# Optimization experiments

Hardware: AMD Instinct MI355X
Metric: run time of the kernel (lower is better)

## Reference

```python
import jax, jax.numpy as jnp
import numpy as np

B, S, D, FF, E = 4, 2048, 1024, 4096, 8


def setup_inputs() -> dict:
    key = jax.random.key(0)
    ks = jax.random.split(key, 6)
    scale_r = 1.0 / np.sqrt(D)
    return {
        "x": jax.random.normal(ks[0], (B, S, D), dtype=jnp.float32),
        "W_router": jax.random.normal(ks[1], (D, E), dtype=jnp.float32) * scale_r,
        "W1": jax.random.normal(ks[2], (E, D, FF), dtype=jnp.float32) * (1.0 / np.sqrt(D)),
        "b1": jnp.zeros((E, FF), dtype=jnp.float32),
        "W2": jax.random.normal(ks[3], (E, FF, D), dtype=jnp.float32) * (1.0 / np.sqrt(FF)),
        "b2": jnp.zeros((E, D), dtype=jnp.float32),
    }


def reference(x, W_router, W1, b1, W2, b2):
    # Router: softmax over experts, top-2, renormalize the 2 gates with softmax
    logits = jnp.einsum("bsd,de->bse", x, W_router)          # [B,S,E]
    probs = jax.nn.softmax(logits, axis=-1)
    top_vals, top_idx = jax.lax.top_k(probs, 2)               # [B,S,2]
    gates2 = jax.nn.softmax(top_vals, axis=-1)                # [B,S,2]

    num_experts = W1.shape[0]
    out = jnp.zeros_like(x)
    # Faithful masked-dense MoE: each expert runs over all tokens (input masked),
    # output scaled by its gate (0 for non-selected tokens).
    for i in range(num_experts):
        sel = (top_idx == i)                                  # [B,S,2] bool
        mask = jnp.any(sel, axis=-1, keepdims=True).astype(x.dtype)  # [B,S,1]
        xi = x * mask
        h = jax.nn.gelu(jnp.einsum("bsd,df->bsf", xi, W1[i]) + b1[i], approximate=False)
        yi = jnp.einsum("bsf,fd->bsd", h, W2[i]) + b2[i]
        g = jnp.sum(gates2 * sel.astype(x.dtype), axis=-1, keepdims=True)  # [B,S,1]
        out = out + yi * g
    return out
```

## Files before the change

### kernel.cpp

```cpp
#include <hip/hip_runtime.h>
#include <hip/hip_bf16.h>
#include <math.h>

#define NEXP 8
#define DDIM 1024
#define FFDIM 4096
#define NTOK 8192
#define NSLOT (NTOK * 2)
#define BM 128
#define BN 128
#define BK 64
#define MAXT ((NSLOT / BM) + NEXP)

typedef __attribute__((ext_vector_type(8))) __bf16 bf16x8;
typedef __attribute__((ext_vector_type(4))) __bf16 bf16x4;
typedef __attribute__((ext_vector_type(4))) float f32x4;

union BF8 { __bf16 b[8]; uint4 u; bf16x8 v; };

typedef const __attribute__((address_space(1))) void* gptr1_t;
typedef __attribute__((address_space(3))) void* lptr3_t;
__device__ __forceinline__ void gll16(const void* g, void* l) {
    __builtin_amdgcn_global_load_lds((gptr1_t)g, (lptr3_t)l, 16, 0, 0);
}

__device__ __forceinline__ float gelu_fast(float v) {
    float vv = v * v;
    float ex = __expf(v * fmaf(0.0713548162726f, vv, 1.59576912161f));
    float s = __builtin_amdgcn_rcpf(ex + 1.0f);
    return v * (1.0f - s);
}

__device__ __forceinline__ int swz(int row, int colb) {
    return row * 128 + (colb ^ ((row & 7) << 4));
}

__device__ __forceinline__ int xcd_logical(int bid, int nwg) {
    if (nwg & 7) return bid;
    return (bid & 7) * (nwg >> 3) + (bid >> 3);
}

__global__ __launch_bounds__(256)
void router_kernel(const float* __restrict__ x, const float* __restrict__ Wr,
                   __bf16* __restrict__ xb, int write_xb,
                   int* __restrict__ idx2, float* __restrict__ gates2,
                   int* __restrict__ counts)
{
    int tid = threadIdx.x;
    int t = blockIdx.x * 4 + (tid >> 6);
    int lane = tid & 63;
    const float* xr = x + (size_t)t * DDIM;

    float acc[NEXP];
#pragma unroll
    for (int e = 0; e < NEXP; ++e) acc[e] = 0.f;

#pragma unroll
    for (int i = 0; i < 2; ++i) {
        int d0 = i * 512 + lane * 8;
        float4 a = *(const float4*)(xr + d0);
        float4 b = *(const float4*)(xr + d0 + 4);
        float vals[8] = {a.x, a.y, a.z, a.w, b.x, b.y, b.z, b.w};
#pragma unroll
        for (int q = 0; q < 8; ++q) {
            const float* wrow = Wr + (size_t)(d0 + q) * NEXP;
#pragma unroll
            for (int e = 0; e < NEXP; ++e) acc[e] += vals[q] * wrow[e];
        }
        if (write_xb) {
            BF8 pk;
#pragma unroll
            for (int q = 0; q < 8; ++q) pk.b[q] = (__bf16)vals[q];
            *(uint4*)(xb + (size_t)t * DDIM + d0) = pk.u;
        }
    }
#pragma unroll
    for (int e = 0; e < NEXP; ++e) {
        float v = acc[e];
        for (int off = 32; off > 0; off >>= 1) v += __shfl_xor(v, off, 64);
        acc[e] = v;
    }
    if (lane == 0) {
        float mx = acc[0];
#pragma unroll
        for (int e = 1; e < NEXP; ++e) mx = fmaxf(mx, acc[e]);
        float p[NEXP]; float s = 0.f;
#pragma unroll
        for (int e = 0; e < NEXP; ++e) { p[e] = expf(acc[e] - mx); s += p[e]; }
        float inv = 1.f / s;
#pragma unroll
        for (int e = 0; e < NEXP; ++e) p[e] *= inv;
        int i1 = 0; float p1 = p[0];
#pragma unroll
        for (int e = 1; e < NEXP; ++e) if (p[e] > p1) { p1 = p[e]; i1 = e; }
        int i2 = -1; float p2 = -1.f;
#pragma unroll
        for (int e = 0; e < NEXP; ++e) {
            if (e == i1) continue;
            if (p[e] > p2) { p2 = p[e]; i2 = e; }
        }
        float u = expf(p2 - p1);
        float den = 1.f + u;
        idx2[2 * t] = i1; idx2[2 * t + 1] = i2;
        gates2[2 * t] = 1.f / den; gates2[2 * t + 1] = u / den;
        atomicAdd(&counts[i1], 1);
        atomicAdd(&counts[i2], 1);
    }
}

__global__ __launch_bounds__(256)
void offsets_kernel(const int* __restrict__ counts, int* __restrict__ offsets,
                    int* __restrict__ cursors, int* __restrict__ tiletab)
{
    __shared__ int soff[NEXP], stile[NEXP + 1];
    int tid = threadIdx.x;
    if (tid == 0) {
        int off = 0, tt = 0;
        for (int e = 0; e < NEXP; ++e) {
            soff[e] = off; stile[e] = tt;
            int c = counts[e];
            off += c; tt += (c + BM - 1) / BM;
        }
        stile[NEXP] = tt;
    }
    __syncthreads();
    if (tid < NEXP) { offsets[tid] = soff[tid]; cursors[tid] = 0; }
    int total = stile[NEXP];
    for (int i = tid; i < MAXT; i += 256) {
        if (i < total) {
            int e = 0;
            while (stile[e + 1] <= i) ++e;
            tiletab[2 * i] = e; tiletab[2 * i + 1] = i - stile[e];
        } else {
            tiletab[2 * i] = -1; tiletab[2 * i + 1] = 0;
        }
    }
}

__global__ __launch_bounds__(256)
void fill_kernel(const int* __restrict__ idx2, const float* __restrict__ gates2,
                 const int* __restrict__ offsets, int* __restrict__ cursors,
                 int* __restrict__ perm, float* __restrict__ gate_slot,
                 int* __restrict__ tslot)
{
    int t = blockIdx.x * 256 + threadIdx.x;
    if (t >= NTOK) return;
#pragma unroll
    for (int s = 0; s < 2; ++s) {
        int e = idx2[2 * t + s];
        int pos = atomicAdd(&cursors[e], 1);
        int slot = offsets[e] + pos;
        perm[slot] = t;
        gate_slot[slot] = gates2[2 * t + s];
        tslot[2 * t + s] = slot;
    }
}

__global__ __launch_bounds__(256)
void convert_w_kernel(const float* __restrict__ W1, const float* __restrict__ W2,
                      __bf16* __restrict__ W1T, __bf16* __restrict__ W2T)
{
    __shared__ float tile[64][133];
    int y = blockIdx.y;
    const float* W; __bf16* WT; int K, N, e;
    if (y < NEXP) { W = W1; WT = W1T; K = DDIM; N = FFDIM; e = y; }
    else          { W = W2; WT = W2T; K = FFDIM; N = DDIM; e = y - NEXP; }
    int ktiles = K >> 6;
    int nt = blockIdx.x / ktiles;
    int kt = blockIdx.x % ktiles;
    const float* We = W + (size_t)e * K * N + (size_t)(kt * 64) * N + nt * 128;
    int tid = threadIdx.x;

    int kr = tid >> 5;
    int n4 = (tid & 31) * 4;
#pragma unroll
    for (int i = 0; i < 8; ++i) {
        int k = kr + i * 8;
        float4 v = *(const float4*)(We + (size_t)k * N + n4);
        tile[k][n4] = v.x; tile[k][n4 + 1] = v.y;
        tile[k][n4 + 2] = v.z; tile[k][n4 + 3] = v.w;
    }
    __syncthreads();

    char* dstb = (char*)WT + ((((size_t)e * (N >> 7) + nt) * ktiles + kt) << 14);
#pragma unroll
    for (int it = 0; it < 4; ++it) {
        int off = it * 4096 + tid * 16;
        int r = off >> 7;
        int s = (off >> 4) & 7;
        int gi = s ^ (r & 7);
        BF8 pk;
#pragma unroll
        for (int q = 0; q < 8; ++q) pk.b[q] = (__bf16)tile[gi * 8 + q][r];
        *(uint4*)(dstb + off) = pk.u;
    }
}

__device__ __forceinline__ bool tile_header(const int* counts, const int* offsets,
                                            const int* tiletab, int e_arg, int c_arg, int CH,
                                            int tile_idx,
                                            int& e, int& start, int& cnt, int& hbase, int& row0,
                                            int& rows_here)
{
    int rowtile;
    if (e_arg >= 0) {
        e = e_arg;
        int cbase = c_arg * CH;
        cnt = counts[e] - cbase;
        if (cnt <= 0) return false;
        if (cnt > CH) cnt = CH;
        start = offsets[e] + cbase;
        rowtile = tile_idx;
        hbase = start;
    } else {
        e = tiletab[2 * tile_idx];
        if (e < 0) return false;
        rowtile = tiletab[2 * tile_idx + 1];
        start = offsets[e];
        cnt = counts[e];
        hbase = 0;
    }
    row0 = rowtile * BM;
    if (row0 >= cnt) return false;
    rows_here = cnt - row0;
    if (rows_here > BM) rows_here = BM;
    return true;
}

__global__ __launch_bounds__(256)
void gemm1_fast(const __bf16* __restrict__ xb, const __bf16* __restrict__ W1T,
                const float* __restrict__ b1,
                const int* __restrict__ perm, const int* __restrict__ counts,
                const int* __restrict__ offsets, const int* __restrict__ tiletab,
                __bf16* __restrict__ H, int e_arg, int c_arg, int CH)
{
    __shared__ __align__(16) char smem[(BM + BN) * 128];
    char* As = smem;
    char* Bs = smem + BM * 128;

    int e, start, cnt, hbase, row0, rows_here;
    if (!tile_header(counts, offsets, tiletab, e_arg, c_arg, CH, blockIdx.y,
                     e, start, cnt, hbase, row0, rows_here))
        return;

    const float* b1e = b1 + (size_t)e * FFDIM;
    int nt = blockIdx.x;
    int n0 = nt * BN;
    const char* bsrc = (const char*)W1T + ((((size_t)e * (FFDIM >> 7) + nt) * (DDIM >> 6)) << 14);

    int tid = threadIdx.x;
    int lane = tid & 63;
    int wid = tid >> 6;
    int wm = wid >> 1, wn = wid & 1;
    int lr = lane & 15, lhi = lane >> 4;

    int ar = tid >> 1, ach = tid & 1;
    int token = -1;
    if (ar < rows_here) token = perm[start + row0 + ar];
    const __bf16* arow = xb + (size_t)(token < 0 ? 0 : token) * DDIM + ach * 32;

    const char* bwave = bsrc + wid * 4096 + lane * 16;
    char* bldsb = Bs + wid * 4096;

    f32x4 acc[4][4] = {};

    for (int kt = 0; kt < DDIM / BK; ++kt) {
        __syncthreads();
#pragma unroll
        for (int j = 0; j < 4; ++j)
            gll16(bwave + ((size_t)kt << 14) + j * 1024, bldsb + j * 1024);
        {
            uint4 v[4];
            if (token >= 0) {
                const uint4* p = (const uint4*)(arow + kt * BK);
#pragma unroll
                for (int i = 0; i < 4; ++i) v[i] = p[i];
            } else {
#pragma unroll
                for (int i = 0; i < 4; ++i) v[i] = make_uint4(0u, 0u, 0u, 0u);
            }
#pragma unroll
            for (int i = 0; i < 4; ++i)
                *(uint4*)(As + swz(ar, ach * 64 + i * 16)) = v[i];
        }
        __syncthreads();

#pragma unroll
        for (int kk = 0; kk < 2; ++kk) {
            bf16x8 af[4], bfr[4];
#pragma unroll
            for (int m = 0; m < 4; ++m)
                af[m] = *(const bf16x8*)(As + swz(wm * 64 + m * 16 + lr, kk * 64 + lhi * 16));
#pragma unroll
            for (int n = 0; n < 4; ++n)
                bfr[n] = *(const bf16x8*)(Bs + swz(wn * 64 + n * 16 + lr, kk * 64 + lhi * 16));
#pragma unroll
            for (int m = 0; m < 4; ++m)
#pragma unroll
                for (int n = 0; n < 4; ++n)
                    acc[m][n] = __builtin_amdgcn_mfma_f32_16x16x32_bf16(af[m], bfr[n], acc[m][n], 0, 0, 0);
        }
    }

    float bias[4];
#pragma unroll
    for (int n = 0; n < 4; ++n) bias[n] = b1e[n0 + wn * 64 + n * 16 + lr];

#pragma unroll
    for (int m = 0; m < 4; ++m) {
        int rbase = wm * 64 + m * 16 + lhi * 4;
#pragma unroll
        for (int j = 0; j < 4; ++j) {
            int rl = rbase + j;
            if (rl < rows_here) {
                __bf16* hr = H + (size_t)(start + row0 + rl - hbase) * FFDIM + n0 + wn * 64;
#pragma unroll
                for (int n = 0; n < 4; ++n) {
                    float v = acc[m][n][j] + bias[n];
                    hr[n * 16 + lr] = (__bf16)gelu_fast(v);
                }
            }
        }
    }
}

__global__ __launch_bounds__(256)
void gemm2_fast(const __bf16* __restrict__ H, const __bf16* __restrict__ W2T,
                const float* __restrict__ b2,
                const int* __restrict__ perm, const float* __restrict__ gate_slot,
                const int* __restrict__ counts, const int* __restrict__ offsets,
                const int* __restrict__ tiletab,
                float* __restrict__ out, __bf16* __restrict__ Y, int use_y,
                int e_arg, int c_arg, int CH)
{
    __shared__ __align__(16) char smem[(BM + BN) * 128];
    char* As = smem;
    char* Bs = smem + BM * 128;

    const int NTN = DDIM / BN;
    int tile_idx, nt;
    if (e_arg >= 0) { nt = blockIdx.x; tile_idx = blockIdx.y; }
    else {
        int L = xcd_logical(blockIdx.x, gridDim.x);
        nt = L % NTN;
        tile_idx = L / NTN;
    }

    int e, start, cnt, hbase, row0, rows_here;
    if (!tile_header(counts, offsets, tiletab, e_arg, c_arg, CH, tile_idx,
                     e, start, cnt, hbase, row0, rows_here))
        return;

    const float* b2e = b2 + (size_t)e * DDIM;
    int n0 = nt * BN;
    const char* bsrc = (const char*)W2T + ((((size_t)e * (DDIM >> 7) + nt) * (FFDIM >> 6)) << 14);

    int tid = threadIdx.x;
    int lane = tid & 63;
    int wid = tid >> 6;
    int wm = wid >> 1, wn = wid & 1;
    int lr = lane & 15, lhi = lane >> 4;

    int ar = tid >> 1, ach = tid & 1;
    bool aval = (ar < rows_here);
    const __bf16* hrow = H + (size_t)(aval ? (start + row0 + ar - hbase) : 0) * FFDIM + ach * 32;

    const char* bwave = bsrc + wid * 4096 + lane * 16;
    char* bldsb = Bs + wid * 4096;

    f32x4 acc[4][4] = {};

    for (int kt = 0; kt < FFDIM / BK; ++kt) {
        __syncthreads();
#pragma unroll
        for (int j = 0; j < 4; ++j)
            gll16(bwave + ((size_t)kt << 14) + j * 1024, bldsb + j * 1024);
        {
            uint4 v[4];
            if (aval) {
                const uint4* p = (const uint4*)(hrow + kt * BK);
#pragma unroll
                for (int i = 0; i < 4; ++i) v[i] = p[i];
            } else {
#pragma unroll
                for (int i = 0; i < 4; ++i) v[i] = make_uint4(0u, 0u, 0u, 0u);
            }
#pragma unroll
            for (int i = 0; i < 4; ++i)
                *(uint4*)(As + swz(ar, ach * 64 + i * 16)) = v[i];
        }
        __syncthreads();

#pragma unroll
        for (int kk = 0; kk < 2; ++kk) {
            bf16x8 af[4], bfr[4];
#pragma unroll
            for (int m = 0; m < 4; ++m)
                af[m] = *(const bf16x8*)(As + swz(wm * 64 + m * 16 + lr, kk * 64 + lhi * 16));
#pragma unroll
            for (int n = 0; n < 4; ++n)
                bfr[n] = *(const bf16x8*)(Bs + swz(wn * 64 + n * 16 + lr, kk * 64 + lhi * 16));
#pragma unroll
            for (int m = 0; m < 4; ++m)
#pragma unroll
                for (int n = 0; n < 4; ++n)
                    acc[m][n] = __builtin_amdgcn_mfma_f32_16x16x32_bf16(af[m], bfr[n], acc[m][n], 0, 0, 0);
        }
    }

    float bias[4];
#pragma unroll
    for (int n = 0; n < 4; ++n) bias[n] = b2e[n0 + wn * 64 + n * 16 + lr];

#pragma unroll
    for (int m = 0; m < 4; ++m) {
        int rbase = wm * 64 + m * 16 + lhi * 4;
#pragma unroll
        for (int j = 0; j < 4; ++j) {
            int rl = rbase + j;
            if (rl < rows_here) {
                int slot = start + row0 + rl;
                float g = gate_slot[slot];
                if (use_y) {
                    __bf16* yrow = Y + (size_t)slot * DDIM + n0 + wn * 64;
#pragma unroll
                    for (int n = 0; n < 4; ++n)
                        yrow[n * 16 + lr] = (__bf16)((acc[m][n][j] + bias[n]) * g);
                } else {
                    int token = perm[slot];
                    float* orow = out + (size_t)token * DDIM + n0 + wn * 64;
#pragma unroll
                    for (int n = 0; n < 4; ++n)
                        atomicAdd(orow + n * 16 + lr, (acc[m][n][j] + bias[n]) * g);
                }
            }
        }
    }
}

__global__ __launch_bounds__(256)
void combine_kernel(const __bf16* __restrict__ Y, const int* __restrict__ tslot,
                    float* __restrict__ out)
{
    int t = blockIdx.x;
    int c = threadIdx.x * 4;
    int sa = tslot[2 * t], sb = tslot[2 * t + 1];
    bf16x4 a = *(const bf16x4*)(Y + (size_t)sa * DDIM + c);
    bf16x4 b = *(const bf16x4*)(Y + (size_t)sb * DDIM + c);
    float4 r;
    r.x = (float)a[0] + (float)b[0];
    r.y = (float)a[1] + (float)b[1];
    r.z = (float)a[2] + (float)b[2];
    r.w = (float)a[3] + (float)b[3];
    *(float4*)(out + (size_t)t * DDIM + c) = r;
}

__global__ __launch_bounds__(256)
void gemm1_legacy(const float* __restrict__ x, const float* __restrict__ W1,
                  const float* __restrict__ b1,
                  const int* __restrict__ perm, const int* __restrict__ counts,
                  const int* __restrict__ offsets, const int* __restrict__ tiletab,
                  __bf16* __restrict__ H, int e_arg, int c_arg, int CH)
{
    __shared__ __align__(16) char smem[(BM + BN) * 128];
    char* As = smem;
    char* Bs = smem + BM * 128;

    int e, start, cnt, hbase, row0, rows_here;
    if (!tile_header(counts, offsets, tiletab, e_arg, c_arg, CH, blockIdx.y,
                     e, start, cnt, hbase, row0, rows_here))
        return;

    const float* W1e = W1 + (size_t)e * DDIM * FFDIM;
    const float* b1e = b1 + (size_t)e * FFDIM;
    int n0 = blockIdx.x * BN;

    int tid = threadIdx.x;
    int lane = tid & 63;
    int wid = tid >> 6;
    int wm = wid >> 1, wn = wid & 1;
    int lr = lane & 15, lhi = lane >> 4;

    int ar = tid >> 1, ach = tid & 1;
    int token = -1;
    if (ar < rows_here) token = perm[start + row0 + ar];
    const float* arow = x + (size_t)(token < 0 ? 0 : token) * DDIM + ach * 32;

    int bn = tid & 127, bkh = tid >> 7;
    const float* bcol = W1e + (size_t)bkh * 32 * FFDIM + n0 + bn;

    f32x4 acc[4][4] = {};

    for (int k0 = 0; k0 < DDIM; k0 += BK) {
        __syncthreads();
        {
            BF8 pk[4];
            if (token >= 0) {
                const float4* p = (const float4*)(arow + k0);
#pragma unroll
                for (int i = 0; i < 4; ++i) {
                    float4 v0 = p[2 * i], v1 = p[2 * i + 1];
                    pk[i].b[0] = (__bf16)v0.x; pk[i].b[1] = (__bf16)v0.y;
                    pk[i].b[2] = (__bf16)v0.z; pk[i].b[3] = (__bf16)v0.w;
                    pk[i].b[4] = (__bf16)v1.x; pk[i].b[5] = (__bf16)v1.y;
                    pk[i].b[6] = (__bf16)v1.z; pk[i].b[7] = (__bf16)v1.w;
                }
            } else {
#pragma unroll
                for (int i = 0; i < 4; ++i) pk[i].u = make_uint4(0u, 0u, 0u, 0u);
            }
#pragma unroll
            for (int i = 0; i < 4; ++i)
                *(uint4*)(As + swz(ar, ach * 64 + i * 16)) = pk[i].u;
        }
        {
            float f[32];
            const float* p = bcol + (size_t)k0 * FFDIM;
#pragma unroll
            for (int j = 0; j < 32; ++j) f[j] = p[(size_t)j * FFDIM];
#pragma unroll
            for (int i = 0; i < 4; ++i) {
                BF8 pk;
#pragma unroll
                for (int q = 0; q < 8; ++q) pk.b[q] = (__bf16)f[i * 8 + q];
                *(uint4*)(Bs + swz(bn, bkh * 64 + i * 16)) = pk.u;
            }
        }
        __syncthreads();

#pragma unroll
        for (int kk = 0; kk < 2; ++kk) {
            bf16x8 af[4], bfr[4];
#pragma unroll
            for (int m = 0; m < 4; ++m)
                af[m] = *(const bf16x8*)(As + swz(wm * 64 + m * 16 + lr, kk * 64 + lhi * 16));
#pragma unroll
            for (int n = 0; n < 4; ++n)
                bfr[n] = *(const bf16x8*)(Bs + swz(wn * 64 + n * 16 + lr, kk * 64 + lhi * 16));
#pragma unroll
            for (int m = 0; m < 4; ++m)
#pragma unroll
                for (int n = 0; n < 4; ++n)
                    acc[m][n] = __builtin_amdgcn_mfma_f32_16x16x32_bf16(af[m], bfr[n], acc[m][n], 0, 0, 0);
        }
    }

    float bias[4];
#pragma unroll
    for (int n = 0; n < 4; ++n) bias[n] = b1e[n0 + wn * 64 + n * 16 + lr];

#pragma unroll
    for (int m = 0; m < 4; ++m) {
        int rbase = wm * 64 + m * 16 + lhi * 4;
#pragma unroll
        for (int j = 0; j < 4; ++j) {
            int rl = rbase + j;
            if (rl < rows_here) {
                __bf16* hr = H + (size_t)(start + row0 + rl - hbase) * FFDIM + n0 + wn * 64;
#pragma unroll
                for (int n = 0; n < 4; ++n) {
                    float v = acc[m][n][j] + bias[n];
                    hr[n * 16 + lr] = (__bf16)gelu_fast(v);
                }
            }
        }
    }
}

__global__ __launch_bounds__(256)
void gemm2_legacy(const __bf16* __restrict__ H, const float* __restrict__ W2,
                  const float* __restrict__ b2,
                  const int* __restrict__ perm, const float* __restrict__ gate_slot,
                  const int* __restrict__ counts, const int* __restrict__ offsets,
                  const int* __restrict__ tiletab,
                  float* __restrict__ out, int e_arg, int c_arg, int CH)
{
    __shared__ __align__(16) char smem[(BM + BN) * 128];
    char* As = smem;
    char* Bs = smem + BM * 128;

    int e, start, cnt, hbase, row0, rows_here;
    if (!tile_header(counts, offsets, tiletab, e_arg, c_arg, CH, blockIdx.y,
                     e, start, cnt, hbase, row0, rows_here))
        return;

    const float* W2e = W2 + (size_t)e * FFDIM * DDIM;
    const float* b2e = b2 + (size_t)e * DDIM;
    int n0 = blockIdx.x * BN;

    int tid = threadIdx.x;
    int lane = tid & 63;
    int wid = tid >> 6;
    int wm = wid >> 1, wn = wid & 1;
    int lr = lane & 15, lhi = lane >> 4;

    int ar = tid >> 1, ach = tid & 1;
    bool aval = (ar < rows_here);
    const __bf16* hrow = H + (size_t)(aval ? (start + row0 + ar - hbase) : 0) * FFDIM + ach * 32;

    int bn = tid & 127, bkh = tid >> 7;
    const float* bcol = W2e + (size_t)bkh * 32 * DDIM + n0 + bn;

    f32x4 acc[4][4] = {};

    for (int k0 = 0; k0 < FFDIM; k0 += BK) {
        __syncthreads();
        {
            uint4 v[4];
            if (aval) {
                const uint4* p = (const uint4*)(hrow + k0);
#pragma unroll
                for (int i = 0; i < 4; ++i) v[i] = p[i];
            } else {
#pragma unroll
                for (int i = 0; i < 4; ++i) v[i] = make_uint4(0u, 0u, 0u, 0u);
            }
#pragma unroll
            for (int i = 0; i < 4; ++i)
                *(uint4*)(As + swz(ar, ach * 64 + i * 16)) = v[i];
        }
        {
            float f[32];
            const float* p = bcol + (size_t)k0 * DDIM;
#pragma unroll
            for (int j = 0; j < 32; ++j) f[j] = p[(size_t)j * DDIM];
#pragma unroll
            for (int i = 0; i < 4; ++i) {
                BF8 pk;
#pragma unroll
                for (int q = 0; q < 8; ++q) pk.b[q] = (__bf16)f[i * 8 + q];
                *(uint4*)(Bs + swz(bn, bkh * 64 + i * 16)) = pk.u;
            }
        }
        __syncthreads();

#pragma unroll
        for (int kk = 0; kk < 2; ++kk) {
            bf16x8 af[4], bfr[4];
#pragma unroll
            for (int m = 0; m < 4; ++m)
                af[m] = *(const bf16x8*)(As + swz(wm * 64 + m * 16 + lr, kk * 64 + lhi * 16));
#pragma unroll
            for (int n = 0; n < 4; ++n)
                bfr[n] = *(const bf16x8*)(Bs + swz(wn * 64 + n * 16 + lr, kk * 64 + lhi * 16));
#pragma unroll
            for (int m = 0; m < 4; ++m)
#pragma unroll
                for (int n = 0; n < 4; ++n)
                    acc[m][n] = __builtin_amdgcn_mfma_f32_16x16x32_bf16(af[m], bfr[n], acc[m][n], 0, 0, 0);
        }
    }

    float bias[4];
#pragma unroll
    for (int n = 0; n < 4; ++n) bias[n] = b2e[n0 + wn * 64 + n * 16 + lr];

#pragma unroll
    for (int m = 0; m < 4; ++m) {
        int rbase = wm * 64 + m * 16 + lhi * 4;
#pragma unroll
        for (int j = 0; j < 4; ++j) {
            int rl = rbase + j;
            if (rl < rows_here) {
                int slot = start + row0 + rl;
                int token = perm[slot];
                float g = gate_slot[slot];
                float* orow = out + (size_t)token * DDIM + n0 + wn * 64;
#pragma unroll
                for (int n = 0; n < 4; ++n) {
                    float v = (acc[m][n][j] + bias[n]) * g;
                    atomicAdd(orow + n * 16 + lr, v);
                }
            }
        }
    }
}

extern "C" void kernel_launch(void* const* d_in, const int* in_sizes, int n_in,
                              void* d_out, int out_size, void* d_ws, size_t ws_size,
                              hipStream_t stream)
{
    const float* x  = (const float*)d_in[0];
    const float* Wr = (const float*)d_in[1];
    const float* W1 = (const float*)d_in[2];
    const float* b1 = (const float*)d_in[3];
    const float* W2 = (const float*)d_in[4];
    const float* b2 = (const float*)d_in[5];
    float* out = (float*)d_out;

    char* ws = (char*)d_ws;
    int* counts   = (int*)ws;
    int* offsets  = counts + 8;
    int* cursors  = offsets + 8;
    int* tiletab  = cursors + 8;
    int* idx2     = tiletab + 2 * MAXT;
    float* gates2 = (float*)(idx2 + 2 * NTOK);
    int* perm     = (int*)(gates2 + 2 * NTOK);
    float* gate_slot = (float*)(perm + NSLOT);
    int* tslot    = (int*)(gate_slot + NSLOT);
    char* hraw = (char*)(tslot + 2 * NTOK);
    size_t small_end = (((size_t)(hraw - ws)) + 255) & ~(size_t)255;

    __bf16* xb  = (__bf16*)(ws + small_end);
    __bf16* W1T = xb + (size_t)NTOK * DDIM;
    __bf16* W2T = W1T + (size_t)NEXP * DDIM * FFDIM;
    __bf16* Hf  = W2T + (size_t)NEXP * FFDIM * DDIM;
    __bf16* Y   = W1T;
    size_t fast_off = small_end + ((size_t)NTOK * DDIM + 2 * (size_t)NEXP * DDIM * FFDIM) * 2;
    size_t availHf = ws_size > fast_off ? ws_size - fast_off : 0;
    size_t need_H = (size_t)NSLOT * FFDIM * 2;
    bool have_w = availHf >= (size_t)BM * FFDIM * 2 * 8;

    hipMemsetAsync(counts, 0, 8 * sizeof(int), stream);

    router_kernel<<<NTOK / 4, 256, 0, stream>>>(x, Wr, xb, have_w ? 1 : 0,
                                                idx2, gates2, counts);
    if (have_w) {
        convert_w_kernel<<<dim3(512, 2 * NEXP), 256, 0, stream>>>(W1, W2, W1T, W2T);
    }
    offsets_kernel<<<1, 256, 0, stream>>>(counts, offsets, cursors, tiletab);
    fill_kernel<<<NTOK / 256, 256, 0, stream>>>(idx2, gates2, offsets, cursors, perm, gate_slot, tslot);

    if (have_w && availHf >= need_H) {
        dim3 g1(FFDIM / BN, MAXT, 1);
        gemm1_fast<<<g1, 256, 0, stream>>>(xb, W1T, b1, perm, counts, offsets, tiletab, Hf, -1, 0, 0);
        gemm2_fast<<<(DDIM / BN) * MAXT, 256, 0, stream>>>(Hf, W2T, b2, perm, gate_slot, counts,
                                                           offsets, tiletab, out, Y, 1, -1, 0, 0);
        combine_kernel<<<NTOK, 256, 0, stream>>>(Y, tslot, out);
    } else if (have_w) {
        hipMemsetAsync(d_out, 0, (size_t)out_size * sizeof(float), stream);
        long long chl = (long long)((availHf / ((size_t)FFDIM * 2)) / BM) * BM;
        int CH = (int)(chl > 4096 ? 4096 : chl);
        int nchunk = (NSLOT + CH - 1) / CH;
        for (int e = 0; e < NEXP; ++e) {
            for (int c = 0; c < nchunk; ++c) {
                dim3 g1(FFDIM / BN, CH / BM, 1);
                gemm1_fast<<<g1, 256, 0, stream>>>(xb, W1T, b1, perm, counts, offsets, tiletab, Hf, e, c, CH);
                dim3 g2(DDIM / BN, CH / BM, 1);
                gemm2_fast<<<g2, 256, 0, stream>>>(Hf, W2T, b2, perm, gate_slot, counts, offsets, tiletab,
                                                   out, (__bf16*)nullptr, 0, e, c, CH);
            }
        }
    } else {
        hipMemsetAsync(d_out, 0, (size_t)out_size * sizeof(float), stream);
        __bf16* H = (__bf16*)(ws + small_end);
        size_t avail = ws_size > small_end ? ws_size - small_end : 0;
        if (avail >= need_H) {
            dim3 g1(FFDIM / BN, MAXT, 1);
            gemm1_legacy<<<g1, 256, 0, stream>>>(x, W1, b1, perm, counts, offsets, tiletab, H, -1, 0, 0);
            dim3 g2(DDIM / BN, MAXT, 1);
            gemm2_legacy<<<g2, 256, 0, stream>>>(H, W2, b2, perm, gate_slot, counts, offsets, tiletab, out, -1, 0, 0);
        } else {
            long long chl = (long long)((avail / ((size_t)FFDIM * 2)) / BM) * BM;
            int CH = (int)(chl > 2048 ? 2048 : chl);
            if (CH >= BM) {
                int nchunk = (NSLOT + CH - 1) / CH;
                for (int e = 0; e < NEXP; ++e) {
                    for (int c = 0; c < nchunk; ++c) {
                        dim3 g1(FFDIM / BN, CH / BM, 1);
                        gemm1_legacy<<<g1, 256, 0, stream>>>(x, W1, b1, perm, counts, offsets, tiletab, H, e, c, CH);
                        dim3 g2(DDIM / BN, CH / BM, 1);
                        gemm2_legacy<<<g2, 256, 0, stream>>>(H, W2, b2, perm, gate_slot, counts, offsets, tiletab, out, e, c, CH);
                    }
                }
            }
        }
    }
}
```

Measured before the change: 766.6 us.

## Widen fast GEMM tiles to 128x256 with per-wave 128x64 output

Both fast expert GEMMs now compute 128x256 output tiles instead of 128x128. Each wave covers all 128 rows and a 64-column slice, so the A tile is reused across twice as many columns and half as many blocks reload A. The cost is twice the accumulator registers per wave (8x4 MFMA tiles), 48KB of shared memory and fewer blocks in the grid, which may cut occupancy and wave-level parallelism.

```diff
diff --git a/kernel.cpp b/kernel.cpp
--- a/kernel.cpp
+++ b/kernel.cpp
@@ -8,7 +8,7 @@
 #define NTOK 8192
 #define NSLOT (NTOK * 2)
 #define BM 128
-#define BN 128
+#define BN2 256
 #define BK 64
 #define MAXT ((NSLOT / BM) + NEXP)
 
@@ -234,9 +234,9 @@
                 const int* __restrict__ offsets, const int* __restrict__ tiletab,
                 __bf16* __restrict__ H, int e_arg, int c_arg, int CH)
 {
-    __shared__ __align__(16) char smem[(BM + BN) * 128];
+    __shared__ __align__(16) char smem[48 * 1024];
     char* As = smem;
-    char* Bs = smem + BM * 128;
+    char* Bs = smem + 16384;
 
     int e, start, cnt, hbase, row0, rows_here;
     if (!tile_header(counts, offsets, tiletab, e_arg, c_arg, CH, blockIdx.y,
@@ -244,14 +244,16 @@
         return;
 
     const float* b1e = b1 + (size_t)e * FFDIM;
-    int nt = blockIdx.x;
-    int n0 = nt * BN;
-    const char* bsrc = (const char*)W1T + ((((size_t)e * (FFDIM >> 7) + nt) * (DDIM >> 6)) << 14);
+    int ntb = blockIdx.x;
+    int n0 = ntb * BN2;
+    const int ktiles = DDIM >> 6;
+    const char* bpanel = (const char*)W1T +
+        ((((size_t)e * (FFDIM >> 7) + 2 * ntb) * ktiles) << 14);
+    const size_t substride = (size_t)ktiles << 14;
 
     int tid = threadIdx.x;
     int lane = tid & 63;
     int wid = tid >> 6;
-    int wm = wid >> 1, wn = wid & 1;
     int lr = lane & 15, lhi = lane >> 4;
 
     int ar = tid >> 1, ach = tid & 1;
@@ -259,16 +261,19 @@
     if (ar < rows_here) token = perm[start + row0 + ar];
     const __bf16* arow = xb + (size_t)(token < 0 ? 0 : token) * DDIM + ach * 32;
 
-    const char* bwave = bsrc + wid * 4096 + lane * 16;
-    char* bldsb = Bs + wid * 4096;
-
-    f32x4 acc[4][4] = {};
+    int bsub = wid >> 1;
+    const char* bsrcw = bpanel + bsub * substride + (wid & 1) * 8192 + lane * 16;
+    char* bldsw = Bs + wid * 8192;
+    const char* bfrag = Bs + bsub * 16384;
+    int bro = (wid & 1) * 64;
+
+    f32x4 acc[8][4] = {};
 
     for (int kt = 0; kt < DDIM / BK; ++kt) {
         __syncthreads();
 #pragma unroll
-        for (int j = 0; j < 4; ++j)
-            gll16(bwave + ((size_t)kt << 14) + j * 1024, bldsb + j * 1024);
+        for (int j = 0; j < 8; ++j)
+            gll16(bsrcw + ((size_t)kt << 14) + j * 1024, bldsw + j * 1024);
         {
             uint4 v[4];
             if (token >= 0) {
@@ -287,33 +292,32 @@
 
 #pragma unroll
         for (int kk = 0; kk < 2; ++kk) {
-            bf16x8 af[4], bfr[4];
-#pragma unroll
-            for (int m = 0; m < 4; ++m)
-                af[m] = *(const bf16x8*)(As + swz(wm * 64 + m * 16 + lr, kk * 64 + lhi * 16));
+            bf16x8 bfr[4];
 #pragma unroll
             for (int n = 0; n < 4; ++n)
-                bfr[n] = *(const bf16x8*)(Bs + swz(wn * 64 + n * 16 + lr, kk * 64 + lhi * 16));
-#pragma unroll
-            for (int m = 0; m < 4; ++m)
+                bfr[n] = *(const bf16x8*)(bfrag + swz(bro + n * 16 + lr, kk * 64 + lhi * 16));
+#pragma unroll
+            for (int m = 0; m < 8; ++m) {
+                bf16x8 af = *(const bf16x8*)(As + swz(m * 16 + lr, kk * 64 + lhi * 16));
 #pragma unroll
                 for (int n = 0; n < 4; ++n)
-                    acc[m][n] = __builtin_amdgcn_mfma_f32_16x16x32_bf16(af[m], bfr[n], acc[m][n], 0, 0, 0);
+                    acc[m][n] = __builtin_amdgcn_mfma_f32_16x16x32_bf16(af, bfr[n], acc[m][n], 0, 0, 0);
+            }
         }
     }
 
     float bias[4];
 #pragma unroll
-    for (int n = 0; n < 4; ++n) bias[n] = b1e[n0 + wn * 64 + n * 16 + lr];
-
-#pragma unroll
-    for (int m = 0; m < 4; ++m) {
-        int rbase = wm * 64 + m * 16 + lhi * 4;
+    for (int n = 0; n < 4; ++n) bias[n] = b1e[n0 + wid * 64 + n * 16 + lr];
+
+#pragma unroll
+    for (int m = 0; m < 8; ++m) {
+        int rbase = m * 16 + lhi * 4;
 #pragma unroll
         for (int j = 0; j < 4; ++j) {
             int rl = rbase + j;
             if (rl < rows_here) {
-                __bf16* hr = H + (size_t)(start + row0 + rl - hbase) * FFDIM + n0 + wn * 64;
+                __bf16* hr = H + (size_t)(start + row0 + rl - hbase) * FFDIM + n0 + wid * 64;
 #pragma unroll
                 for (int n = 0; n < 4; ++n) {
                     float v = acc[m][n][j] + bias[n];
@@ -333,16 +337,16 @@
                 float* __restrict__ out, __bf16* __restrict__ Y, int use_y,
                 int e_arg, int c_arg, int CH)
 {
-    __shared__ __align__(16) char smem[(BM + BN) * 128];
+    __shared__ __align__(16) char smem[48 * 1024];
     char* As = smem;
-    char* Bs = smem + BM * 128;
-
-    const int NTN = DDIM / BN;
-    int tile_idx, nt;
-    if (e_arg >= 0) { nt = blockIdx.x; tile_idx = blockIdx.y; }
+    char* Bs = smem + 16384;
+
+    const int NTN = DDIM / BN2;
+    int tile_idx, ntb;
+    if (e_arg >= 0) { ntb = blockIdx.x; tile_idx = blockIdx.y; }
     else {
         int L = xcd_logical(blockIdx.x, gridDim.x);
-        nt = L % NTN;
+        ntb = L % NTN;
         tile_idx = L / NTN;
     }
 
@@ -352,29 +356,34 @@
         return;
 
     const float* b2e = b2 + (size_t)e * DDIM;
-    int n0 = nt * BN;
-    const char* bsrc = (const char*)W2T + ((((size_t)e * (DDIM >> 7) + nt) * (FFDIM >> 6)) << 14);
+    int n0 = ntb * BN2;
+    const int ktiles = FFDIM >> 6;
+    const char* bpanel = (const char*)W2T +
+        ((((size_t)e * (DDIM >> 7) + 2 * ntb) * ktiles) << 14);
+    const size_t substride = (size_t)ktiles << 14;
 
     int tid = threadIdx.x;
     int lane = tid & 63;
     int wid = tid >> 6;
-    int wm = wid >> 1, wn = wid & 1;
     int lr = lane & 15, lhi = lane >> 4;
 
     int ar = tid >> 1, ach = tid & 1;
     bool aval = (ar < rows_here);
     const __bf16* hrow = H + (size_t)(aval ? (start + row0 + ar - hbase) : 0) * FFDIM + ach * 32;
 
-    const char* bwave = bsrc + wid * 4096 + lane * 16;
-    char* bldsb = Bs + wid * 4096;
-
-    f32x4 acc[4][4] = {};
+    int bsub = wid >> 1;
+    const char* bsrcw = bpanel + bsub * substride + (wid & 1) * 8192 + lane * 16;
+    char* bldsw = Bs + wid * 8192;
+    const char* bfrag = Bs + bsub * 16384;
+    int bro = (wid & 1) * 64;
+
+    f32x4 acc[8][4] = {};
 
     for (int kt = 0; kt < FFDIM / BK; ++kt) {
         __syncthreads();
 #pragma unroll
-        for (int j = 0; j < 4; ++j)
-            gll16(bwave + ((size_t)kt << 14) + j * 1024, bldsb + j * 1024);
+        for (int j = 0; j < 8; ++j)
+            gll16(bsrcw + ((size_t)kt << 14) + j * 1024, bldsw + j * 1024);
         {
             uint4 v[4];
             if (aval) {
@@ -393,28 +402,27 @@
 
 #pragma unroll
         for (int kk = 0; kk < 2; ++kk) {
-            bf16x8 af[4], bfr[4];
-#pragma unroll
-            for (int m = 0; m < 4; ++m)
-                af[m] = *(const bf16x8*)(As + swz(wm * 64 + m * 16 + lr, kk * 64 + lhi * 16));
+            bf16x8 bfr[4];
 #pragma unroll
             for (int n = 0; n < 4; ++n)
-                bfr[n] = *(const bf16x8*)(Bs + swz(wn * 64 + n * 16 + lr, kk * 64 + lhi * 16));
-#pragma unroll
-            for (int m = 0; m < 4; ++m)
+                bfr[n] = *(const bf16x8*)(bfrag + swz(bro + n * 16 + lr, kk * 64 + lhi * 16));
+#pragma unroll
+            for (int m = 0; m < 8; ++m) {
+                bf16x8 af = *(const bf16x8*)(As + swz(m * 16 + lr, kk * 64 + lhi * 16));
 #pragma unroll
                 for (int n = 0; n < 4; ++n)
-                    acc[m][n] = __builtin_amdgcn_mfma_f32_16x16x32_bf16(af[m], bfr[n], acc[m][n], 0, 0, 0);
+                    acc[m][n] = __builtin_amdgcn_mfma_f32_16x16x32_bf16(af, bfr[n], acc[m][n], 0, 0, 0);
+            }
         }
     }
 
     float bias[4];
 #pragma unroll
-    for (int n = 0; n < 4; ++n) bias[n] = b2e[n0 + wn * 64 + n * 16 + lr];
-
-#pragma unroll
-    for (int m = 0; m < 4; ++m) {
-        int rbase = wm * 64 + m * 16 + lhi * 4;
+    for (int n = 0; n < 4; ++n) bias[n] = b2e[n0 + wid * 64 + n * 16 + lr];
+
+#pragma unroll
+    for (int m = 0; m < 8; ++m) {
+        int rbase = m * 16 + lhi * 4;
 #pragma unroll
         for (int j = 0; j < 4; ++j) {
             int rl = rbase + j;
@@ -422,13 +430,13 @@
                 int slot = start + row0 + rl;
                 float g = gate_slot[slot];
                 if (use_y) {
-                    __bf16* yrow = Y + (size_t)slot * DDIM + n0 + wn * 64;
+                    __bf16* yrow = Y + (size_t)slot * DDIM + n0 + wid * 64;
 #pragma unroll
                     for (int n = 0; n < 4; ++n)
                         yrow[n * 16 + lr] = (__bf16)((acc[m][n][j] + bias[n]) * g);
                 } else {
                     int token = perm[slot];
-                    float* orow = out + (size_t)token * DDIM + n0 + wn * 64;
+                    float* orow = out + (size_t)token * DDIM + n0 + wid * 64;
 #pragma unroll
                     for (int n = 0; n < 4; ++n)
                         atomicAdd(orow + n * 16 + lr, (acc[m][n][j] + bias[n]) * g);
@@ -462,7 +470,7 @@
                   const int* __restrict__ offsets, const int* __restrict__ tiletab,
                   __bf16* __restrict__ H, int e_arg, int c_arg, int CH)
 {
-    __shared__ __align__(16) char smem[(BM + BN) * 128];
+    __shared__ __align__(16) char smem[(BM + 128) * 128];
     char* As = smem;
     char* Bs = smem + BM * 128;
 
@@ -473,7 +481,7 @@
 
     const float* W1e = W1 + (size_t)e * DDIM * FFDIM;
     const float* b1e = b1 + (size_t)e * FFDIM;
-    int n0 = blockIdx.x * BN;
+    int n0 = blockIdx.x * 128;
 
     int tid = threadIdx.x;
     int lane = tid & 63;
@@ -575,7 +583,7 @@
                   const int* __restrict__ tiletab,
                   float* __restrict__ out, int e_arg, int c_arg, int CH)
 {
-    __shared__ __align__(16) char smem[(BM + BN) * 128];
+    __shared__ __align__(16) char smem[(BM + 128) * 128];
     char* As = smem;
     char* Bs = smem + BM * 128;
 
@@ -586,7 +594,7 @@
 
     const float* W2e = W2 + (size_t)e * FFDIM * DDIM;
     const float* b2e = b2 + (size_t)e * DDIM;
-    int n0 = blockIdx.x * BN;
+    int n0 = blockIdx.x * 128;
 
     int tid = threadIdx.x;
     int lane = tid & 63;
@@ -722,10 +730,10 @@
     fill_kernel<<<NTOK / 256, 256, 0, stream>>>(idx2, gates2, offsets, cursors, perm, gate_slot, tslot);
 
     if (have_w && availHf >= need_H) {
-        dim3 g1(FFDIM / BN, MAXT, 1);
+        dim3 g1(FFDIM / BN2, MAXT, 1);
         gemm1_fast<<<g1, 256, 0, stream>>>(xb, W1T, b1, perm, counts, offsets, tiletab, Hf, -1, 0, 0);
-        gemm2_fast<<<(DDIM / BN) * MAXT, 256, 0, stream>>>(Hf, W2T, b2, perm, gate_slot, counts,
-                                                           offsets, tiletab, out, Y, 1, -1, 0, 0);
+        gemm2_fast<<<(DDIM / BN2) * MAXT, 256, 0, stream>>>(Hf, W2T, b2, perm, gate_slot, counts,
+                                                            offsets, tiletab, out, Y, 1, -1, 0, 0);
         combine_kernel<<<NTOK, 256, 0, stream>>>(Y, tslot, out);
     } else if (have_w) {
         hipMemsetAsync(d_out, 0, (size_t)out_size * sizeof(float), stream);
@@ -734,9 +742,9 @@
         int nchunk = (NSLOT + CH - 1) / CH;
         for (int e = 0; e < NEXP; ++e) {
             for (int c = 0; c < nchunk; ++c) {
-                dim3 g1(FFDIM / BN, CH / BM, 1);
+                dim3 g1(FFDIM / BN2, CH / BM, 1);
                 gemm1_fast<<<g1, 256, 0, stream>>>(xb, W1T, b1, perm, counts, offsets, tiletab, Hf, e, c, CH);
-                dim3 g2(DDIM / BN, CH / BM, 1);
+                dim3 g2(DDIM / BN2, CH / BM, 1);
                 gemm2_fast<<<g2, 256, 0, stream>>>(Hf, W2T, b2, perm, gate_slot, counts, offsets, tiletab,
                                                    out, (__bf16*)nullptr, 0, e, c, CH);
             }
@@ -746,9 +754,9 @@
         __bf16* H = (__bf16*)(ws + small_end);
         size_t avail = ws_size > small_end ? ws_size - small_end : 0;
         if (avail >= need_H) {
-            dim3 g1(FFDIM / BN, MAXT, 1);
+            dim3 g1(FFDIM / 128, MAXT, 1);
             gemm1_legacy<<<g1, 256, 0, stream>>>(x, W1, b1, perm, counts, offsets, tiletab, H, -1, 0, 0);
-            dim3 g2(DDIM / BN, MAXT, 1);
+            dim3 g2(DDIM / 128, MAXT, 1);
             gemm2_legacy<<<g2, 256, 0, stream>>>(H, W2, b2, perm, gate_slot, counts, offsets, tiletab, out, -1, 0, 0);
         } else {
             long long chl = (long long)((avail / ((size_t)FFDIM * 2)) / BM) * BM;
@@ -757,9 +765,9 @@
                 int nchunk = (NSLOT + CH - 1) / CH;
                 for (int e = 0; e < NEXP; ++e) {
                     for (int c = 0; c < nchunk; ++c) {
-                        dim3 g1(FFDIM / BN, CH / BM, 1);
+                        dim3 g1(FFDIM / 128, CH / BM, 1);
                         gemm1_legacy<<<g1, 256, 0, stream>>>(x, W1, b1, perm, counts, offsets, tiletab, H, e, c, CH);
-                        dim3 g2(DDIM / BN, CH / BM, 1);
+                        dim3 g2(DDIM / 128, CH / BM, 1);
                         gemm2_legacy<<<g2, 256, 0, stream>>>(H, W2, b2, perm, gate_slot, counts, offsets, tiletab, out, e, c, CH);
                     }
                 }
```

Result: slower. 1.117 ms (+45.7%).
